# Optimization experiments

Measured on AMD Instinct MI355X. Metric: run time of the kernel, lower is better.

The kernel has to match this reference:

```python
import jax, jax.numpy as jnp
import numpy as np

D_MODEL = 1024
D_HIDDEN = 4096
NUM_EXPERT = 2
TOP_K = 1
W_SCALE = 0.02  # keep expert pre-exp outputs small so exp() in combine stays finite
EPS = float(np.finfo(float).eps)


def setup_inputs() -> dict:
    key = jax.random.key(0)
    ks = jax.random.split(key, 6)
    x = jax.random.normal(ks[0], (4, 4096, D_MODEL), dtype=jnp.float32)
    Wg = jax.random.normal(ks[1], (D_MODEL, NUM_EXPERT), dtype=jnp.float32) * W_SCALE
    bg = jax.random.normal(ks[2], (NUM_EXPERT,), dtype=jnp.float32) * W_SCALE
    We = jax.random.normal(ks[3], (NUM_EXPERT, D_MODEL, D_HIDDEN), dtype=jnp.float32) * W_SCALE
    be = jax.random.normal(ks[4], (NUM_EXPERT, D_HIDDEN), dtype=jnp.float32) * W_SCALE
    return {"x": x, "Wg": Wg, "bg": bg, "We": We, "be": be}


def reference(x, Wg, bg, We, be):
    B, N, C = x.shape
    xt = x.reshape(-1, C)                               # [T, C]
    # NaiveGate: linear -> top-k -> softmax over top-k logits -> dense scatter
    logits = xt @ Wg + bg                               # [T, E]
    top_v, top_i = jax.lax.top_k(logits, TOP_K)         # [T, k]
    top_g = jax.nn.softmax(top_v, axis=-1)              # [T, k] (==1.0 when k=1)
    gates = jnp.sum(jax.nn.one_hot(top_i, NUM_EXPERT, dtype=logits.dtype) * top_g[..., None], axis=1)  # [T, E]
    # expert FFNs (dense over all tokens; gate==0 tokens contribute nothing in combine,
    # matching SparseDispatcher semantics exactly)
    eo = jnp.einsum('tc,ech->eth', xt, We) + be[:, None, :]   # [E, T, H]
    # combine: sum_e gate[t,e] * exp(expert_e(x_t)); zeros -> eps; then log
    combined = jnp.einsum('te,eth->th', gates, jnp.exp(eo))   # [T, H]
    combined = jnp.where(combined == 0, EPS, combined)
    return jnp.log(combined).reshape(B, N, D_HIDDEN)
```

## Files before the change

### kernel.cpp

```cpp
#include <hip/hip_runtime.h>
#include <hip/hip_bf16.h>


#define DM 1024
#define DH 4096
#define KS 32
#define NS (DM / KS)

typedef __attribute__((ext_vector_type(4))) float f32x4;
typedef __attribute__((ext_vector_type(8))) __bf16 bf16x8;

__device__ __forceinline__ unsigned short f2bf(float f) {
    union { float f; unsigned u; } a; a.f = f;
    unsigned u = a.u;
    u += 0x7fffu + ((u >> 16) & 1u);
    return (unsigned short)(u >> 16);
}

__device__ __forceinline__ void gl16(const unsigned short* g, unsigned short* l) {
    __builtin_amdgcn_global_load_lds(
        (const __attribute__((address_space(1))) unsigned int*)(g),
        (__attribute__((address_space(3))) unsigned int*)(l), 16, 0, 0);
}

__global__ __launch_bounds__(1024) void prep(
    const float* __restrict__ x, const float* __restrict__ Wg,
    const float* __restrict__ bg, const float* __restrict__ We, int T,
    unsigned short* __restrict__ xbf, unsigned short* __restrict__ webt,
    int* __restrict__ perm, int* __restrict__ eidx, int* __restrict__ cur)
{
    int bid = blockIdx.x, tid = threadIdx.x;

    if (bid < 512) {
        __shared__ unsigned short tile[4][64][72];
        int sub = tid >> 8, t2 = tid & 255;
        int g = bid * 4 + sub;
        int e = g >> 10, rr = g & 1023, kt = rr >> 6, ht = rr & 63;
        int k0 = kt * 64, h0 = ht * 64;
        int k = t2 >> 2, hc = t2 & 3;
        const float* src = We + ((size_t)e * DM + k0 + k) * DH + h0 + hc * 16;
#pragma unroll
        for (int j = 0; j < 4; ++j) {
            f32x4 v = *(const f32x4*)(src + j * 4);
#pragma unroll
            for (int q = 0; q < 4; ++q)
                tile[sub][hc * 16 + j * 4 + q][k] = f2bf(v[q]);
        }
        __syncthreads();
        int h = t2 >> 2, kc = t2 & 3;
        unsigned short* dst = webt + ((size_t)e * DH + h0 + h) * DM + k0 + kc * 16;
        *(uint4*)(dst)     = *(const uint4*)&tile[sub][h][kc * 16];
        *(uint4*)(dst + 8) = *(const uint4*)&tile[sub][h][kc * 16 + 8];
        return;
    }

    __shared__ unsigned char eL[64];
    int gb = bid - 512;
    int lane = tid & 63, w = tid >> 6;
    float wgv[32];
#pragma unroll
    for (int j = 0; j < 8; ++j)
        *(f32x4*)&wgv[j * 4] = *(const f32x4*)(Wg + lane * 32 + j * 4);
    float bg0 = bg[0], bg1 = bg[1];
    int t0 = gb * 64 + w * 4;
#pragma unroll
    for (int tl = 0; tl < 4; ++tl) {
        int t = t0 + tl;
        const float* xr = x + (size_t)t * DM + lane * 16;
        double g0 = 0.0, g1 = 0.0;
        unsigned hw[8];
#pragma unroll
        for (int j = 0; j < 4; ++j) {
            f32x4 v = *(const f32x4*)(xr + j * 4);
#pragma unroll
            for (int q = 0; q < 4; ++q) {
                g0 += (double)v[q] * (double)wgv[2 * (j * 4 + q)];
                g1 += (double)v[q] * (double)wgv[2 * (j * 4 + q) + 1];
            }
            hw[j * 2]     = (unsigned)f2bf(v[0]) | ((unsigned)f2bf(v[1]) << 16);
            hw[j * 2 + 1] = (unsigned)f2bf(v[2]) | ((unsigned)f2bf(v[3]) << 16);
        }
        unsigned short* xw = xbf + (size_t)t * DM + lane * 16;
        uint4 u0; u0.x = hw[0]; u0.y = hw[1]; u0.z = hw[2]; u0.w = hw[3];
        uint4 u1; u1.x = hw[4]; u1.y = hw[5]; u1.z = hw[6]; u1.w = hw[7];
        *(uint4*)(xw)     = u0;
        *(uint4*)(xw + 8) = u1;
#pragma unroll
        for (int off = 32; off; off >>= 1) {
            g0 += __shfl_xor(g0, off);
            g1 += __shfl_xor(g1, off);
        }
        if (lane == 0) {
            int ee = ((g1 + (double)bg1) > (g0 + (double)bg0)) ? 1 : 0;
            eidx[t] = ee;
            eL[w * 4 + tl] = (unsigned char)ee;
        }
    }
    __syncthreads();
    if (w == 0) {
        int myE = eL[lane];
        unsigned long long m1 = __ballot(myE != 0);
        int tot1 = __popcll(m1);
        int b0 = 0, b1 = 0;
        if (lane == 0) {
            b0 = atomicAdd(cur, 64 - tot1);
            b1 = atomicAdd(cur + 1, tot1);
        }
        b0 = __shfl(b0, 0);
        b1 = __shfl(b1, 0);
        unsigned long long lm = (1ull << lane) - 1ull;
        int rank = __popcll((myE ? m1 : ~m1) & lm);
        int dstp = myE ? (T - b1 - tot1 + rank) : (b0 + rank);
        perm[dstp] = gb * 64 + lane;
    }
}

__global__ __launch_bounds__(256, 3) void moe_gemm(
    const unsigned short* __restrict__ xbf,
    const unsigned short* __restrict__ webt,
    const float* __restrict__ be,
    const int* __restrict__ perm,
    const int* __restrict__ eidx,
    float* __restrict__ out)
{
    __shared__ __align__(16) char smem[3 * 16384];

    const int nwg = gridDim.x;
    const int bid = blockIdx.x;
    const int swz = (bid & 7) * (nwg >> 3) + (bid >> 3);
    const int mt = swz >> 5, nt = swz & 31;
    const int m0 = mt * 128, n0 = nt * 128;
    const int tid = threadIdx.x, lane = tid & 63, wid = tid >> 6;
    const int wm = wid >> 1, wn = wid & 1;

    const unsigned short *aptr0, *aptr1;
    size_t bofs0, bofs1;
    {
        int c0 = tid, c1 = tid + 256;
        int r0 = c0 >> 2, k80 = (c0 & 3) ^ ((r0 >> 1) & 3);
        int r1 = c1 >> 2, k81 = (c1 & 3) ^ ((r1 >> 1) & 3);
        aptr0 = xbf + (size_t)perm[m0 + r0] * DM + k80 * 8;
        aptr1 = xbf + (size_t)perm[m0 + r1] * DM + k81 * 8;
        bofs0 = (size_t)(n0 + r0) * DM + k80 * 8;
        bofs1 = (size_t)(n0 + r1) * DM + k81 * 8;
    }

    const int rA = wm * 64 + (lane & 15);
    const int rB = wn * 64 + (lane & 15);
    const int offA = rA * KS + (((lane >> 4) ^ ((rA >> 1) & 3)) * 8);
    const int offB = rB * KS + (((lane >> 4) ^ ((rB >> 1) & 3)) * 8);

    const int e_lo = eidx[perm[m0]];
    const int e_hi = eidx[perm[m0 + 127]];

    for (int e = e_lo; e <= e_hi; ++e) {
        const unsigned short* wb = webt + (size_t)e * DH * DM;

        __syncthreads();

#pragma unroll
        for (int s = 0; s < 2; ++s) {
            unsigned short* Asl = (unsigned short*)(smem + s * 16384);
            unsigned short* Bsl = (unsigned short*)(smem + s * 16384 + 8192);
            gl16(aptr0 + s * KS, Asl + tid * 8);
            gl16(aptr1 + s * KS, Asl + (tid + 256) * 8);
            gl16(wb + bofs0 + s * KS, Bsl + tid * 8);
            gl16(wb + bofs1 + s * KS, Bsl + (tid + 256) * 8);
        }

        f32x4 acc[4][4];
#pragma unroll
        for (int mi = 0; mi < 4; ++mi)
#pragma unroll
            for (int ni = 0; ni < 4; ++ni) acc[mi][ni] = 0.f;

        asm volatile("s_waitcnt vmcnt(4)" ::: "memory");
        __builtin_amdgcn_s_barrier();

        unsigned o_cur = 0, o_nxt = 16384, o_pf = 32768;
#pragma unroll 1
        for (int kt = 0; kt < NS; ++kt) {
            if (kt + 2 < NS) {
                unsigned short* Asl = (unsigned short*)(smem + o_pf);
                unsigned short* Bsl = (unsigned short*)(smem + o_pf + 8192);
                gl16(aptr0 + (kt + 2) * KS, Asl + tid * 8);
                gl16(aptr1 + (kt + 2) * KS, Asl + (tid + 256) * 8);
                gl16(wb + bofs0 + (kt + 2) * KS, Bsl + tid * 8);
                gl16(wb + bofs1 + (kt + 2) * KS, Bsl + (tid + 256) * 8);
            }
            __builtin_amdgcn_sched_barrier(0);

            const unsigned short* As = (const unsigned short*)(smem + o_cur);
            const unsigned short* Bs = (const unsigned short*)(smem + o_cur + 8192);
            bf16x8 af[4], bfr[4];
#pragma unroll
            for (int mi = 0; mi < 4; ++mi) af[mi] = *(const bf16x8*)(As + offA + mi * 16 * KS);
#pragma unroll
            for (int ni = 0; ni < 4; ++ni) bfr[ni] = *(const bf16x8*)(Bs + offB + ni * 16 * KS);
#pragma unroll
            for (int mi = 0; mi < 4; ++mi)
#pragma unroll
                for (int ni = 0; ni < 4; ++ni)
                    acc[mi][ni] = __builtin_amdgcn_mfma_f32_16x16x32_bf16(
                        af[mi], bfr[ni], acc[mi][ni], 0, 0, 0);

            __builtin_amdgcn_sched_barrier(0);
            if (kt < NS - 2) asm volatile("s_waitcnt vmcnt(4)" ::: "memory");
            else             asm volatile("s_waitcnt vmcnt(0)" ::: "memory");
            __builtin_amdgcn_s_barrier();
            __builtin_amdgcn_sched_barrier(0);

            unsigned t = o_cur; o_cur = o_nxt; o_nxt = o_pf; o_pf = t;
        }

        float* ep = (float*)smem + wid * (16 * 68);
        const int colb = n0 + wn * 64;
        float bev[4];
#pragma unroll
        for (int ni = 0; ni < 4; ++ni) bev[ni] = be[e * DH + colb + ni * 16 + (lane & 15)];
        const bool multi = (e_lo != e_hi);
        const int rowb = m0 + wm * 64;

#pragma unroll
        for (int mi = 0; mi < 4; ++mi) {
#pragma unroll
            for (int ni = 0; ni < 4; ++ni)
#pragma unroll
                for (int r = 0; r < 4; ++r)
                    ep[((lane >> 4) * 4 + r) * 68 + ni * 16 + (lane & 15)] =
                        acc[mi][ni][r] + bev[ni];
#pragma unroll
            for (int g = 0; g < 4; ++g) {
                f32x4 v = *(const f32x4*)&ep[(g * 4 + (lane >> 4)) * 68 + (lane & 15) * 4];
                int tk = perm[rowb + mi * 16 + g * 4 + (lane >> 4)];
                if (!multi || eidx[tk] == e)
                    __builtin_nontemporal_store(
                        v, (f32x4*)(out + (size_t)tk * DH + colb + (lane & 15) * 4));
            }
        }
    }
}

extern "C" void kernel_launch(void* const* d_in, const int* in_sizes, int n_in,
                              void* d_out, int out_size, void* d_ws, size_t ws_size,
                              hipStream_t stream) {
    const float* x  = (const float*)d_in[0];
    const float* Wg = (const float*)d_in[1];
    const float* bg = (const float*)d_in[2];
    const float* We = (const float*)d_in[3];
    const float* be = (const float*)d_in[4];
    float* out = (float*)d_out;
    int T = in_sizes[0] / DM;

    char* ws = (char*)d_ws;
    int* cur  = (int*)ws;
    int* perm = (int*)(ws + 4096);
    int* eidx = (int*)(ws + 4096 + 65536);
    unsigned short* webt = (unsigned short*)(ws + 4096 + 2 * 65536);
    unsigned short* xbf  = (unsigned short*)(ws + 4096 + 2 * 65536 + (size_t)2 * DH * DM * 2);

    hipMemsetAsync(cur, 0, 8, stream);
    hipLaunchKernelGGL(prep, dim3(512 + T / 64), dim3(1024), 0, stream,
                       x, Wg, bg, We, T, xbf, webt, perm, eidx, cur);
    int nblk = (T / 128) * (DH / 128);
    hipLaunchKernelGGL(moe_gemm, dim3(nblk), dim3(256), 0, stream,
                       xbf, webt, be, perm, eidx, out);
}
```

Measured before the change: 232.7 us.

## Enlarge GEMM tile to 256x256 with 512 threads and XCD-aware block mapping

The grouped GEMM tile grows from 128x128 with 4 waves to 256x256 with 8 waves, each wave computing 128x64. LDS stages grow to 32KB each, three-deep. A new block-to-tile mapping for the 1024-block grid keeps neighbouring tiles on the same XCD to improve L2 reuse. The larger tile halves global loads per FLOP but raises register pressure (128 accumulator floats per lane), limits occupancy to 2 blocks, and spends more work on mixed-expert tiles.

```diff
diff --git a/kernel.cpp b/kernel.cpp
--- a/kernel.cpp
+++ b/kernel.cpp
@@ -6,6 +6,8 @@
 #define DH 4096
 #define KS 32
 #define NS (DM / KS)
+#define SLOT (256 * KS)
+#define SLOTB (SLOT * 4)
 
 typedef __attribute__((ext_vector_type(4))) float f32x4;
 typedef __attribute__((ext_vector_type(8))) __bf16 bf16x8;
@@ -115,7 +117,7 @@
     }
 }
 
-__global__ __launch_bounds__(256, 3) void moe_gemm(
+__global__ __launch_bounds__(512, 2) void moe_gemm(
     const unsigned short* __restrict__ xbf,
     const unsigned short* __restrict__ webt,
     const float* __restrict__ be,
@@ -123,35 +125,43 @@
     const int* __restrict__ eidx,
     float* __restrict__ out)
 {
-    __shared__ __align__(16) char smem[3 * 16384];
-
-    const int nwg = gridDim.x;
+    __shared__ __align__(16) char smem[3 * SLOTB];
+
     const int bid = blockIdx.x;
-    const int swz = (bid & 7) * (nwg >> 3) + (bid >> 3);
-    const int mt = swz >> 5, nt = swz & 31;
-    const int m0 = mt * 128, n0 = nt * 128;
+    int mt, nt;
+    if (gridDim.x == 1024) {
+        int xcd = bid & 7, idx = bid >> 3;
+        int mtb = (xcd >> 1) * 16, ntb = (xcd & 1) * 8;
+        int st = idx >> 5, q = idx & 31;
+        mt = mtb + (st >> 1) * 8 + (q >> 2);
+        nt = ntb + (st & 1) * 4 + (q & 3);
+    } else {
+        int swz = (bid & 7) * (gridDim.x >> 3) + (bid >> 3);
+        mt = swz / (DH / 256); nt = swz % (DH / 256);
+    }
+    const int m0 = mt * 256, n0 = nt * 256;
     const int tid = threadIdx.x, lane = tid & 63, wid = tid >> 6;
-    const int wm = wid >> 1, wn = wid & 1;
-
-    const unsigned short *aptr0, *aptr1;
-    size_t bofs0, bofs1;
-    {
-        int c0 = tid, c1 = tid + 256;
-        int r0 = c0 >> 2, k80 = (c0 & 3) ^ ((r0 >> 1) & 3);
-        int r1 = c1 >> 2, k81 = (c1 & 3) ^ ((r1 >> 1) & 3);
-        aptr0 = xbf + (size_t)perm[m0 + r0] * DM + k80 * 8;
-        aptr1 = xbf + (size_t)perm[m0 + r1] * DM + k81 * 8;
-        bofs0 = (size_t)(n0 + r0) * DM + k80 * 8;
-        bofs1 = (size_t)(n0 + r1) * DM + k81 * 8;
-    }
-
-    const int rA = wm * 64 + (lane & 15);
+    const int wm = wid >> 2, wn = wid & 3;
+
+    const unsigned short* aptr[2];
+    size_t bofs[2];
+    unsigned lofs[2];
+#pragma unroll
+    for (int j = 0; j < 2; ++j) {
+        int c = wid * 128 + j * 64 + lane;
+        int row = c >> 2, k8 = (c & 3) ^ ((row >> 1) & 3);
+        aptr[j] = xbf + (size_t)perm[m0 + row] * DM + k8 * 8;
+        bofs[j] = (size_t)(n0 + row) * DM + k8 * 8;
+        lofs[j] = (unsigned)(wid * 128 + j * 64) * 8;
+    }
+
+    const int rA = wm * 128 + (lane & 15);
     const int rB = wn * 64 + (lane & 15);
     const int offA = rA * KS + (((lane >> 4) ^ ((rA >> 1) & 3)) * 8);
     const int offB = rB * KS + (((lane >> 4) ^ ((rB >> 1) & 3)) * 8);
 
     const int e_lo = eidx[perm[m0]];
-    const int e_hi = eidx[perm[m0 + 127]];
+    const int e_hi = eidx[perm[m0 + 255]];
 
     for (int e = e_lo; e <= e_hi; ++e) {
         const unsigned short* wb = webt + (size_t)e * DH * DM;
@@ -160,45 +170,47 @@
 
 #pragma unroll
         for (int s = 0; s < 2; ++s) {
-            unsigned short* Asl = (unsigned short*)(smem + s * 16384);
-            unsigned short* Bsl = (unsigned short*)(smem + s * 16384 + 8192);
-            gl16(aptr0 + s * KS, Asl + tid * 8);
-            gl16(aptr1 + s * KS, Asl + (tid + 256) * 8);
-            gl16(wb + bofs0 + s * KS, Bsl + tid * 8);
-            gl16(wb + bofs1 + s * KS, Bsl + (tid + 256) * 8);
-        }
-
-        f32x4 acc[4][4];
-#pragma unroll
-        for (int mi = 0; mi < 4; ++mi)
+            unsigned short* Asl = (unsigned short*)(smem + s * SLOTB);
+            unsigned short* Bsl = (unsigned short*)(smem + s * SLOTB) + SLOT;
+#pragma unroll
+            for (int j = 0; j < 2; ++j) {
+                gl16(aptr[j] + s * KS, Asl + lofs[j]);
+                gl16(wb + bofs[j] + s * KS, Bsl + lofs[j]);
+            }
+        }
+
+        f32x4 acc[8][4];
+#pragma unroll
+        for (int mi = 0; mi < 8; ++mi)
 #pragma unroll
             for (int ni = 0; ni < 4; ++ni) acc[mi][ni] = 0.f;
 
         asm volatile("s_waitcnt vmcnt(4)" ::: "memory");
         __builtin_amdgcn_s_barrier();
 
-        unsigned o_cur = 0, o_nxt = 16384, o_pf = 32768;
+        unsigned o_cur = 0, o_nxt = SLOTB, o_pf = 2 * SLOTB;
 #pragma unroll 1
         for (int kt = 0; kt < NS; ++kt) {
             if (kt + 2 < NS) {
                 unsigned short* Asl = (unsigned short*)(smem + o_pf);
-                unsigned short* Bsl = (unsigned short*)(smem + o_pf + 8192);
-                gl16(aptr0 + (kt + 2) * KS, Asl + tid * 8);
-                gl16(aptr1 + (kt + 2) * KS, Asl + (tid + 256) * 8);
-                gl16(wb + bofs0 + (kt + 2) * KS, Bsl + tid * 8);
-                gl16(wb + bofs1 + (kt + 2) * KS, Bsl + (tid + 256) * 8);
+                unsigned short* Bsl = (unsigned short*)(smem + o_pf) + SLOT;
+#pragma unroll
+                for (int j = 0; j < 2; ++j) {
+                    gl16(aptr[j] + (kt + 2) * KS, Asl + lofs[j]);
+                    gl16(wb + bofs[j] + (kt + 2) * KS, Bsl + lofs[j]);
+                }
             }
             __builtin_amdgcn_sched_barrier(0);
 
             const unsigned short* As = (const unsigned short*)(smem + o_cur);
-            const unsigned short* Bs = (const unsigned short*)(smem + o_cur + 8192);
-            bf16x8 af[4], bfr[4];
-#pragma unroll
-            for (int mi = 0; mi < 4; ++mi) af[mi] = *(const bf16x8*)(As + offA + mi * 16 * KS);
+            const unsigned short* Bs = (const unsigned short*)(smem + o_cur) + SLOT;
+            bf16x8 af[8], bfr[4];
+#pragma unroll
+            for (int mi = 0; mi < 8; ++mi) af[mi] = *(const bf16x8*)(As + offA + mi * 16 * KS);
 #pragma unroll
             for (int ni = 0; ni < 4; ++ni) bfr[ni] = *(const bf16x8*)(Bs + offB + ni * 16 * KS);
 #pragma unroll
-            for (int mi = 0; mi < 4; ++mi)
+            for (int mi = 0; mi < 8; ++mi)
 #pragma unroll
                 for (int ni = 0; ni < 4; ++ni)
                     acc[mi][ni] = __builtin_amdgcn_mfma_f32_16x16x32_bf16(
@@ -213,25 +225,25 @@
             unsigned t = o_cur; o_cur = o_nxt; o_nxt = o_pf; o_pf = t;
         }
 
-        float* ep = (float*)smem + wid * (16 * 68);
+        float* ep = (float*)smem + wid * (16 * 72);
         const int colb = n0 + wn * 64;
         float bev[4];
 #pragma unroll
         for (int ni = 0; ni < 4; ++ni) bev[ni] = be[e * DH + colb + ni * 16 + (lane & 15)];
         const bool multi = (e_lo != e_hi);
-        const int rowb = m0 + wm * 64;
-
-#pragma unroll
-        for (int mi = 0; mi < 4; ++mi) {
+        const int rowb = m0 + wm * 128;
+
+#pragma unroll
+        for (int mi = 0; mi < 8; ++mi) {
 #pragma unroll
             for (int ni = 0; ni < 4; ++ni)
 #pragma unroll
                 for (int r = 0; r < 4; ++r)
-                    ep[((lane >> 4) * 4 + r) * 68 + ni * 16 + (lane & 15)] =
+                    ep[((lane >> 4) * 4 + r) * 72 + ni * 16 + (lane & 15)] =
                         acc[mi][ni][r] + bev[ni];
 #pragma unroll
             for (int g = 0; g < 4; ++g) {
-                f32x4 v = *(const f32x4*)&ep[(g * 4 + (lane >> 4)) * 68 + (lane & 15) * 4];
+                f32x4 v = *(const f32x4*)&ep[(g * 4 + (lane >> 4)) * 72 + (lane & 15) * 4];
                 int tk = perm[rowb + mi * 16 + g * 4 + (lane >> 4)];
                 if (!multi || eidx[tk] == e)
                     __builtin_nontemporal_store(
@@ -262,7 +274,7 @@
     hipMemsetAsync(cur, 0, 8, stream);
     hipLaunchKernelGGL(prep, dim3(512 + T / 64), dim3(1024), 0, stream,
                        x, Wg, bg, We, T, xbf, webt, perm, eidx, cur);
-    int nblk = (T / 128) * (DH / 128);
-    hipLaunchKernelGGL(moe_gemm, dim3(nblk), dim3(256), 0, stream,
+    int nblk = (T / 256) * (DH / 256);
+    hipLaunchKernelGGL(moe_gemm, dim3(nblk), dim3(512), 0, stream,
                        xbf, webt, be, perm, eidx, out);
 }
```

Result: faster. 215.0 us (-7.6%).

## Deepen GEMM pipeline with register double-buffering and tile-grouped XCD swizzle

Applied to the files above, without the earlier changes.

Restructures the K loop to prefetch three LDS stages ahead and to load the next step's MFMA fragments into a second register set while the current step's MFMAs run, with raised wave priority around the MFMA block. Block-to-tile mapping is also changed so each XCD works on contiguous 8x4 groups of tiles for better L2 reuse of A and B. The aim is to hide LDS read latency and global load latency behind the matrix math. In exchange it uses more registers (two fragment sets) under the 3-blocks-per-SM launch bound, and the waitcnt/barrier ordering becomes more delicate.

```diff
diff --git a/kernel.cpp b/kernel.cpp
--- a/kernel.cpp
+++ b/kernel.cpp
@@ -125,10 +125,11 @@
 {
     __shared__ __align__(16) char smem[3 * 16384];
 
-    const int nwg = gridDim.x;
     const int bid = blockIdx.x;
-    const int swz = (bid & 7) * (nwg >> 3) + (bid >> 3);
-    const int mt = swz >> 5, nt = swz & 31;
+    const int xcd = bid & 7, idx = bid >> 3;
+    const int st = idx >> 5, q = idx & 31;
+    const int mt = xcd * 16 + (st >> 3) * 8 + (q >> 2);
+    const int nt = (st & 7) * 4 + (q & 3);
     const int m0 = mt * 128, n0 = nt * 128;
     const int tid = threadIdx.x, lane = tid & 63, wid = tid >> 6;
     const int wm = wid >> 1, wn = wid & 1;
@@ -159,7 +160,7 @@
         __syncthreads();
 
 #pragma unroll
-        for (int s = 0; s < 2; ++s) {
+        for (int s = 0; s < 3; ++s) {
             unsigned short* Asl = (unsigned short*)(smem + s * 16384);
             unsigned short* Bsl = (unsigned short*)(smem + s * 16384 + 8192);
             gl16(aptr0 + s * KS, Asl + tid * 8);
@@ -177,42 +178,58 @@
         asm volatile("s_waitcnt vmcnt(4)" ::: "memory");
         __builtin_amdgcn_s_barrier();
 
-        unsigned o_cur = 0, o_nxt = 16384, o_pf = 32768;
-#pragma unroll 1
-        for (int kt = 0; kt < NS; ++kt) {
-            if (kt + 2 < NS) {
-                unsigned short* Asl = (unsigned short*)(smem + o_pf);
-                unsigned short* Bsl = (unsigned short*)(smem + o_pf + 8192);
-                gl16(aptr0 + (kt + 2) * KS, Asl + tid * 8);
-                gl16(aptr1 + (kt + 2) * KS, Asl + (tid + 256) * 8);
-                gl16(wb + bofs0 + (kt + 2) * KS, Bsl + tid * 8);
-                gl16(wb + bofs1 + (kt + 2) * KS, Bsl + (tid + 256) * 8);
-            }
-            __builtin_amdgcn_sched_barrier(0);
-
-            const unsigned short* As = (const unsigned short*)(smem + o_cur);
-            const unsigned short* Bs = (const unsigned short*)(smem + o_cur + 8192);
-            bf16x8 af[4], bfr[4];
-#pragma unroll
-            for (int mi = 0; mi < 4; ++mi) af[mi] = *(const bf16x8*)(As + offA + mi * 16 * KS);
-#pragma unroll
-            for (int ni = 0; ni < 4; ++ni) bfr[ni] = *(const bf16x8*)(Bs + offB + ni * 16 * KS);
+        bf16x8 fa0[4], fb0[4], fa1[4], fb1[4];
+        {
+            const unsigned short* As = (const unsigned short*)(smem);
+            const unsigned short* Bs = (const unsigned short*)(smem + 8192);
+#pragma unroll
+            for (int mi = 0; mi < 4; ++mi) fa0[mi] = *(const bf16x8*)(As + offA + mi * 16 * KS);
+#pragma unroll
+            for (int ni = 0; ni < 4; ++ni) fb0[ni] = *(const bf16x8*)(Bs + offB + ni * 16 * KS);
+        }
+
+        auto step = [&](int kt, bf16x8 (&ca)[4], bf16x8 (&cb)[4],
+                        bf16x8 (&na)[4], bf16x8 (&nb)[4]) {
+            if (kt + 3 < NS) {
+                int sl = kt % 3;
+                unsigned short* Asl = (unsigned short*)(smem + sl * 16384);
+                unsigned short* Bsl = (unsigned short*)(smem + sl * 16384 + 8192);
+                gl16(aptr0 + (kt + 3) * KS, Asl + tid * 8);
+                gl16(aptr1 + (kt + 3) * KS, Asl + (tid + 256) * 8);
+                gl16(wb + bofs0 + (kt + 3) * KS, Bsl + tid * 8);
+                gl16(wb + bofs1 + (kt + 3) * KS, Bsl + (tid + 256) * 8);
+            }
+            if (kt + 1 < NS) {
+                int sl = (kt + 1) % 3;
+                const unsigned short* As = (const unsigned short*)(smem + sl * 16384);
+                const unsigned short* Bs = (const unsigned short*)(smem + sl * 16384 + 8192);
+#pragma unroll
+                for (int mi = 0; mi < 4; ++mi) na[mi] = *(const bf16x8*)(As + offA + mi * 16 * KS);
+#pragma unroll
+                for (int ni = 0; ni < 4; ++ni) nb[ni] = *(const bf16x8*)(Bs + offB + ni * 16 * KS);
+            }
+            __builtin_amdgcn_s_setprio(1);
 #pragma unroll
             for (int mi = 0; mi < 4; ++mi)
 #pragma unroll
                 for (int ni = 0; ni < 4; ++ni)
                     acc[mi][ni] = __builtin_amdgcn_mfma_f32_16x16x32_bf16(
-                        af[mi], bfr[ni], acc[mi][ni], 0, 0, 0);
-
+                        ca[mi], cb[ni], acc[mi][ni], 0, 0, 0);
+            __builtin_amdgcn_s_setprio(0);
             __builtin_amdgcn_sched_barrier(0);
-            if (kt < NS - 2) asm volatile("s_waitcnt vmcnt(4)" ::: "memory");
-            else             asm volatile("s_waitcnt vmcnt(0)" ::: "memory");
+            if (kt < NS - 3)       asm volatile("s_waitcnt vmcnt(4)" ::: "memory");
+            else if (kt == NS - 3) asm volatile("s_waitcnt vmcnt(0)" ::: "memory");
             __builtin_amdgcn_s_barrier();
             __builtin_amdgcn_sched_barrier(0);
-
-            unsigned t = o_cur; o_cur = o_nxt; o_nxt = o_pf; o_pf = t;
-        }
-
+        };
+
+#pragma unroll 1
+        for (int kt = 0; kt < NS; kt += 2) {
+            step(kt,     fa0, fb0, fa1, fb1);
+            step(kt + 1, fa1, fb1, fa0, fb0);
+        }
+
+        __syncthreads();
         float* ep = (float*)smem + wid * (16 * 68);
         const int colb = n0 + wn * 64;
         float bev[4];
```

Measured after the change: 209.1 us. -10.1%, faster.
